# Optimization experiments

Measured on AMD Instinct MI355X. Metric: run time of the kernel, lower is better.

## Reference

```python
import jax, jax.numpy as jnp
import numpy as np

EPS = 1e-5

def conv2d(x, w, b, stride, pad):
    out = jax.lax.conv_general_dilated(x, w, (stride, stride), [(pad, pad), (pad, pad)],
                                       dimension_numbers=('NCHW', 'OIHW', 'NCHW'))
    return out + b[None, :, None, None]

def instance_norm(x):
    # nn.InstanceNorm2d default: affine=False, eps=1e-5, per (N,C) over (H,W)
    m = jnp.mean(x, axis=(2, 3), keepdims=True)
    v = jnp.var(x, axis=(2, 3), keepdims=True)
    return (x - m) * jax.lax.rsqrt(v + EPS)

def deform_conv2d(x, offset, mask, w, b, stride, pad):
    # x: [N,Cin,H,W]; offset: [N,2K,Ho,Wo] as [dy(K);dx(K)]; mask: [N,K,Ho,Wo]
    N, Cin, H, W = x.shape
    Cout, _, kh, kw = w.shape
    K = kh * kw
    Ho, Wo = mask.shape[2], mask.shape[3]
    oy, ox = offset[:, :K], offset[:, K:]
    ky, kx = jnp.meshgrid(jnp.arange(kh), jnp.arange(kw), indexing='ij')
    ky = ky.reshape(K).astype(x.dtype)
    kx = kx.reshape(K).astype(x.dtype)
    base_y = (jnp.arange(Ho) * stride - pad).astype(x.dtype)
    base_x = (jnp.arange(Wo) * stride - pad).astype(x.dtype)
    # sampling coords [N,K,Ho,Wo]
    py = base_y[None, None, :, None] + ky[None, :, None, None] + oy
    px = base_x[None, None, None, :] + kx[None, :, None, None] + ox
    y0 = jnp.floor(py)
    x0 = jnp.floor(px)
    wy = (py - y0)[:, None]  # [N,1,K,Ho,Wo]
    wx = (px - x0)[:, None]
    flat = x.reshape(N, Cin, H * W)

    def sample(yi, xi):
        valid = ((yi >= 0) & (yi <= H - 1) & (xi >= 0) & (xi <= W - 1)).astype(x.dtype)
        yc = jnp.clip(yi, 0, H - 1).astype(jnp.int32)
        xc = jnp.clip(xi, 0, W - 1).astype(jnp.int32)
        idx = yc * W + xc  # [N,K,Ho,Wo]
        vals = jax.vmap(lambda f, i: f[:, i])(flat, idx)  # [N,Cin,K,Ho,Wo]
        return vals * valid[:, None]

    v00 = sample(y0, x0)
    v01 = sample(y0, x0 + 1)
    v10 = sample(y0 + 1, x0)
    v11 = sample(y0 + 1, x0 + 1)
    samp = (v00 * (1 - wy) * (1 - wx) + v01 * (1 - wy) * wx
            + v10 * wy * (1 - wx) + v11 * wy * wx)
    samp = samp * mask[:, None]  # modulated (DCNv2)
    out = jnp.einsum('nckhw,ock->nohw', samp, w.reshape(Cout, Cin, K))
    return out + b[None, :, None, None]

def mdcp(x, off_w, off_b, dcn_w, dcn_b, stride, pad):
    # ModulatedDeformConvPack.forward with input_offset == input_real == x
    o = conv2d(x, off_w, off_b, stride, pad)
    K = o.shape[1] // 3
    o1, o2, m = o[:, :K], o[:, K:2 * K], o[:, 2 * K:]
    offset = jnp.concatenate([o1, o2], axis=1)
    mask = jax.nn.sigmoid(m)
    return deform_conv2d(x, offset, mask, dcn_w, dcn_b, stride, pad)

def res_block(x, w1, b1, w2, b2):
    # MUNIT-style ResBlock: [reflect-pad conv3x3, IN, ReLU] -> [reflect-pad conv3x3, IN] + skip
    h = jnp.pad(x, ((0, 0), (0, 0), (1, 1), (1, 1)), mode='reflect')
    h = jax.nn.relu(instance_norm(conv2d(h, w1, b1, 1, 0)))
    h = jnp.pad(h, ((0, 0), (0, 0), (1, 1), (1, 1)), mode='reflect')
    h = instance_norm(conv2d(h, w2, b2, 1, 0))
    return x + h

def setup_inputs() -> dict:
    key = jax.random.key(0)
    ks = jax.random.split(key, 32)
    N, H, W = 2, 256, 256

    def wconv(k, shape, scale=None):
        if scale is None:
            scale = 1.0 / np.sqrt(shape[1] * shape[2] * shape[3])
        return jax.random.normal(k, shape, jnp.float32) * scale

    def bias(k, n, scale=0.01):
        return jax.random.normal(k, (n,), jnp.float32) * scale

    inp = {}
    inp['x'] = jax.random.normal(ks[0], (N, 3, H, W), jnp.float32)
    # offset/mask convs: small weights (sub-pixel offsets; trained-from-zero in original)
    inp['off1_w'] = wconv(ks[1], (147, 3, 7, 7), 0.01)
    inp['off1_b'] = bias(ks[2], 147)
    inp['dcn1_w'] = wconv(ks[3], (64, 3, 7, 7))
    inp['dcn1_b'] = bias(ks[4], 64)
    inp['off2_w'] = wconv(ks[5], (48, 64, 4, 4), 0.01)
    inp['off2_b'] = bias(ks[6], 48)
    inp['dcn2_w'] = wconv(ks[7], (128, 64, 4, 4))
    inp['dcn2_b'] = bias(ks[8], 128)
    inp['off3_w'] = wconv(ks[9], (48, 128, 4, 4), 0.01)
    inp['off3_b'] = bias(ks[10], 48)
    inp['dcn3_w'] = wconv(ks[11], (256, 128, 4, 4))
    inp['dcn3_b'] = bias(ks[12], 256)
    for i, base in ((1, 13), (2, 17)):
        inp[f'rb{i}_w1'] = wconv(ks[base], (256, 256, 3, 3))
        inp[f'rb{i}_b1'] = bias(ks[base + 1], 256)
        inp[f'rb{i}_w2'] = wconv(ks[base + 2], (256, 256, 3, 3))
        inp[f'rb{i}_b2'] = bias(ks[base + 3], 256)
    return inp

def reference(x, off1_w, off1_b, dcn1_w, dcn1_b, off2_w, off2_b, dcn2_w, dcn2_b,
              off3_w, off3_b, dcn3_w, dcn3_b,
              rb1_w1, rb1_b1, rb1_w2, rb1_b2, rb2_w1, rb2_b1, rb2_w2, rb2_b2):
    h = jax.nn.relu(instance_norm(mdcp(x, off1_w, off1_b, dcn1_w, dcn1_b, 1, 3)))
    skip1 = h
    h = jax.nn.relu(instance_norm(mdcp(h, off2_w, off2_b, dcn2_w, dcn2_b, 2, 1)))
    skip2 = h
    h = jax.nn.relu(instance_norm(mdcp(h, off3_w, off3_b, dcn3_w, dcn3_b, 2, 1)))
    h = res_block(h, rb1_w1, rb1_b1, rb1_w2, rb1_b2)
    h = res_block(h, rb2_w1, rb2_b1, rb2_w2, rb2_b2)
    return (h, skip1, skip2)
```

## Files before the change

kernel.cpp:

```cpp
#include <hip/hip_runtime.h>
#include <hip/hip_bf16.h>
#include <math.h>

#define TPB 256
typedef __hip_bfloat16 bf16;
typedef short bf16x8 __attribute__((ext_vector_type(8)));
typedef float f32x4 __attribute__((ext_vector_type(4)));

constexpr long BIASF  = 0;
constexpr long RB1W1T = 2048;
constexpr long RB1W2T = 591872;
constexpr long RB2W1T = 1181696;
constexpr long RB2W2T = 1771520;
constexpr long FB     = 2361344;
constexpr long WB1OT  = 2361344;
constexpr long WB1DT  = 2382956;
constexpr long WO2T   = 2392364;
constexpr long WB2T   = 2441516;
constexpr long WO3T   = 2572588;
constexpr long WB3T   = 2670892;
constexpr long OFFB   = 3221504;
constexpr long H3F    = 4458496;
constexpr long PSUM   = 5507072;
constexpr long PSQ    = 5515264;
constexpr long CLBUF  = 5523456;
constexpr long OFF1B = 0,   DCN1B = 147;
constexpr long OFF2B = 211, DCN2B = 259;
constexpr long OFF3B = 387, DCN3B = 435;
constexpr long RB1B1 = 691, RB1B2 = 947;
constexpr long RB2B1 = 1203, RB2B2 = 1459;

template<int BF>
__device__ __forceinline__ float ldT(const void* p, long i) {
    if (BF) {
        unsigned short h = ((const unsigned short*)p)[i];
        return __uint_as_float(((unsigned int)h) << 16);
    }
    return ((const float*)p)[i];
}
template<int BF>
__device__ __forceinline__ void stT(void* p, long i, float v) {
    if (BF) ((bf16*)p)[i] = __float2bfloat16(v);
    else    ((float*)p)[i] = v;
}
__device__ __forceinline__ float bitsToF(unsigned short h) {
    return __uint_as_float(((unsigned int)h) << 16);
}
__device__ __forceinline__ unsigned short fToBits(float v) {
    bf16 h = __float2bfloat16(v);
    return *(unsigned short*)&h;
}

__global__ void detect_kernel(const void* __restrict__ x, int* __restrict__ flag) {
    if (threadIdx.x == 0 && blockIdx.x == 0) {
        const unsigned short* u = (const unsigned short*)x;
        int sane = 0;
        for (int i = 0; i < 256; ++i) {
            float v = bitsToF(u[i]);
            float a = fabsf(v);
            if (a > 0.0009f && a < 1100.f) ++sane;
        }
        *flag = (sane >= 224) ? 1 : 0;
    }
}

struct PtrPack { const void* p[20]; };

template<int BF>
__device__ void repack_all_body(PtrPack pp, float* __restrict__ fw)
{
    constexpr int  bcum  [11] = {0,147,211,259,387,435,691,947,1203,1459,1715};
    int j0 = blockIdx.x * 1024 + threadIdx.x * 4;
    #pragma unroll
    for (int q = 0; q < 4; ++q) {
        int j = j0 + q;
        if (j < 1715) {
            int v = 0;
            #pragma unroll
            for (int s = 1; s < 10; ++s) if (j >= bcum[s]) v = s;
            fw[BIASF + j] = ldT<BF>(pp.p[10 + v], j - bcum[v]);
        }
    }
}
__global__ __launch_bounds__(TPB) void repack_all_kernel(
    PtrPack pp, float* fw, const int* dflag) {
    if (*dflag) repack_all_body<1>(pp, fw);
    else        repack_all_body<0>(pp, fw);
}

__global__ __launch_bounds__(TPB) void repack_dcn_kernel(
    const void* __restrict__ w2, const void* __restrict__ w3,
    const void* __restrict__ w1o, const void* __restrict__ w1d,
    const void* __restrict__ w2o, const void* __restrict__ w3o,
    float* __restrict__ fw, const int* __restrict__ dflag)
{
    int bf = *dflag;
    unsigned short* wb2 = (unsigned short*)(fw + WB2T);
    unsigned short* wb3 = (unsigned short*)(fw + WB3T);
    unsigned short* wb1o = (unsigned short*)(fw + WB1OT);
    unsigned short* wb1d = (unsigned short*)(fw + WB1DT);
    unsigned short* wb2o = (unsigned short*)(fw + WO2T);
    unsigned short* wb3o = (unsigned short*)(fw + WO3T);
    int b = blockIdx.x;
    if (b < 128) {
        int e0 = b * 1024 + threadIdx.x * 4;
        #pragma unroll
        for (int j = 0; j < 4; ++j) {
            int e = e0 + j;
            int co = e >> 10, rem = e & 1023, k = rem >> 6, ci = rem & 63;
            long si = ((long)(co * 64 + ci)) * 16 + k;
            float v = bf ? ldT<1>(w2, si) : ldT<0>(w2, si);
            wb2[e] = fToBits(v);
        }
    } else if (b < 640) {
        int e0 = (b - 128) * 1024 + threadIdx.x * 4;
        #pragma unroll
        for (int j = 0; j < 4; ++j) {
            int e = e0 + j;
            int co = e >> 11, rem = e & 2047, k = rem >> 7, ci = rem & 127;
            long si = ((long)(co * 128 + ci)) * 16 + k;
            float v = bf ? ldT<1>(w3, si) : ldT<0>(w3, si);
            wb3[e] = fToBits(v);
        }
    } else if (b < 665) {
        int e0 = (b - 640) * 1024 + threadIdx.x * 4;
        #pragma unroll
        for (int j = 0; j < 4; ++j) {
            int e = e0 + j;
            int co = e / 160, k = e - co * 160;
            float v = 0.f;
            if (co < 147 && k < 147) {
                long si = (long)co * 147 + k;
                v = bf ? ldT<1>(w1o, si) : ldT<0>(w1o, si);
            }
            wb1o[e] = fToBits(v);
        }
    } else if (b < 675) {
        int e0 = (b - 665) * 1024 + threadIdx.x * 4;
        #pragma unroll
        for (int j = 0; j < 4; ++j) {
            int e = e0 + j;
            int co = e / 160, k = e - co * 160;
            float v = 0.f;
            if (k < 147) {
                long si = (long)co * 147 + k;
                v = bf ? ldT<1>(w1d, si) : ldT<0>(w1d, si);
            }
            wb1d[e] = fToBits(v);
        }
    } else if (b < 739) {
        int e0 = (b - 675) * 1024 + threadIdx.x * 4;
        #pragma unroll
        for (int j = 0; j < 4; ++j) {
            int e = e0 + j;
            int co = e >> 10, rem = e & 1023, k = rem >> 6, ci = rem & 63;
            float v = 0.f;
            if (co < 48) {
                long si = ((long)(co * 64 + ci)) * 16 + k;
                v = bf ? ldT<1>(w2o, si) : ldT<0>(w2o, si);
            }
            wb2o[e] = fToBits(v);
        }
    } else {
        int e0 = (b - 739) * 1024 + threadIdx.x * 4;
        #pragma unroll
        for (int j = 0; j < 4; ++j) {
            int e = e0 + j;
            int co = e >> 11, rem = e & 2047, k = rem >> 7, ci = rem & 127;
            float v = 0.f;
            if (co < 48) {
                long si = ((long)(co * 128 + ci)) * 16 + k;
                v = bf ? ldT<1>(w3o, si) : ldT<0>(w3o, si);
            }
            wb3o[e] = fToBits(v);
        }
    }
}

struct RbPack { const void* src[4]; };
__global__ __launch_bounds__(TPB) void repack_rb_kernel(
    RbPack rp, float* fw, const int* dflag)
{
    __shared__ unsigned short lw[4 * 2304];
    int b = blockIdx.x;
    int ten = b >> 6;
    int co0 = (b & 63) * 4;
    const void* src = rp.src[ten];
    const long dstOff[4] = {RB1W1T, RB1W2T, RB2W1T, RB2W2T};
    unsigned short* dst = (unsigned short*)(fw + dstOff[ten]);
    int bf = *dflag;
    int t = threadIdx.x;
    for (int e = t; e < 4 * 2304; e += TPB) {
        int coL = e / 2304, i = e - coL * 2304;
        long si = (long)(co0 + coL) * 2304 + i;
        float v = bf ? ldT<1>(src, si) : ldT<0>(src, si);
        lw[e] = fToBits(v);
    }
    __syncthreads();
    for (int e = t; e < 9216; e += TPB) {
        int ci = e & 255, coL = (e >> 8) & 3, q = e >> 10;
        dst[((long)q * 256 + co0 + coL) * 256 + ci] = lw[coL * 2304 + ci * 9 + q];
    }
}

template<int BF>
__device__ void x_to_cl4_body(const void* __restrict__ x, unsigned short* __restrict__ x4)
{
    long gid = (long)blockIdx.x * TPB + threadIdx.x;
    int n = (int)(gid >> 16); int p = (int)(gid & 65535);
    long xb = (long)n * 3 * 65536 + p;
    unsigned c0 = fToBits(ldT<BF>(x, xb));
    unsigned c1 = fToBits(ldT<BF>(x, xb + 65536));
    unsigned c2 = fToBits(ldT<BF>(x, xb + 131072));
    uint2 v; v.x = c0 | (c1 << 16); v.y = c2;
    *(uint2*)&x4[gid * 4] = v;
}
__global__ __launch_bounds__(TPB) void x_to_cl4_kernel(
    const void* x, unsigned short* x4, const int* dflag)
{
    if (*dflag) x_to_cl4_body<1>(x, x4);
    else        x_to_cl4_body<0>(x, x4);
}

template<int BF>
__device__ void layer1_mfma_body(
    const unsigned short* __restrict__ x4all, const unsigned short* __restrict__ wo,
    const unsigned short* __restrict__ wd, const float* __restrict__ bias1,
    const float* __restrict__ bias2, void* __restrict__ out, long obase,
    float* xs, unsigned short* A, float* offs)
{
    int b = blockIdx.x;
    int n = b >> 11;
    int ho = (b >> 3) & 255;
    int wo0 = (b & 7) << 5;
    const unsigned short* x4 = x4all + ((long)n << 16) * 4;
    int t = threadIdx.x;

    for (int e = t; e < 7 * 40; e += TPB) {
        int cc = e % 40, rr = e / 40;
        int yy = ho - 3 + rr; int xx = wo0 - 3 + cc;
        float c0 = 0.f, c1 = 0.f, c2 = 0.f;
        if (cc < 38 && yy >= 0 && yy < 256 && xx >= 0 && xx < 256) {
            uint2 v = *(const uint2*)&x4[((long)yy * 256 + xx) * 4];
            c0 = bitsToF((unsigned short)(v.x & 0xffff));
            c1 = bitsToF((unsigned short)(v.x >> 16));
            c2 = bitsToF((unsigned short)(v.y & 0xffff));
        }
        xs[(0 * 7 + rr) * 40 + cc] = c0;
        xs[(1 * 7 + rr) * 40 + cc] = c1;
        xs[(2 * 7 + rr) * 40 + cc] = c2;
    }
    __syncthreads();

    for (int e = t; e < 5120; e += TPB) {
        int kin = e & 31, m = (e >> 5) & 31, kc = e >> 10;
        int k = kc * 32 + kin;
        float v = 0.f;
        if (k < 147) {
            int ci = k / 49, q = k - ci * 49;
            int ky = q / 7, kx = q - ky * 7;
            v = xs[(ci * 7 + ky) * 40 + m + kx];
        }
        A[kc * 1024 + m * 32 + kin] = fToBits(v);
    }
    __syncthreads();

    int wv = t >> 6, lane = t & 63;
    int quad = lane >> 4, l16 = lane & 15;
    int mt = wv & 1, ntb = wv >> 1;

    {
        f32x4 acc[5];
        #pragma unroll
        for (int j = 0; j < 5; ++j) acc[j] = (f32x4){0.f, 0.f, 0.f, 0.f};
        #pragma unroll
        for (int kc = 0; kc < 5; ++kc) {
            bf16x8 a = *(const bf16x8*)&A[(kc * 32 + mt * 16 + l16) * 32 + quad * 8];
            #pragma unroll
            for (int j = 0; j < 5; ++j) {
                int ch = (ntb + 2 * j) * 16 + l16;
                bf16x8 bw = *(const bf16x8*)&wo[ch * 160 + kc * 32 + quad * 8];
                acc[j] = __builtin_amdgcn_mfma_f32_16x16x32_bf16(a, bw, acc[j], 0, 0, 0);
            }
        }
        #pragma unroll
        for (int j = 0; j < 5; ++j) {
            int ch = (ntb + 2 * j) * 16 + l16;
            if (ch < 147) {
                float bv = bias1[ch];
                #pragma unroll
                for (int reg = 0; reg < 4; ++reg) {
                    int m = mt * 16 + quad * 4 + reg;
                    offs[ch * 33 + m] = acc[j][reg] + bv;
                }
            }
        }
    }
    __syncthreads();

    for (int e = t; e < 49 * 32; e += TPB) {
        int p = e & 31; int k = e >> 5;
        float oy = offs[k * 33 + p];
        float ox = offs[(49 + k) * 33 + p];
        float mr = offs[(98 + k) * 33 + p];
        float m = 1.f / (1.f + expf(-mr));
        float py = (float)(ho - 3 + k / 7) + oy;
        float px = (float)(wo0 + p - 3 + k % 7) + ox;
        float y0f = floorf(py), x0f = floorf(px);
        float wy = py - y0f, wx = px - x0f;
        int y0 = (int)y0f, x0 = (int)x0f;
        bool yv0 = (y0 >= 0) && (y0 < 256);
        bool yv1 = (y0 + 1 >= 0) && (y0 + 1 < 256);
        bool xv0 = (x0 >= 0) && (x0 < 256);
        bool xv1 = (x0 + 1 >= 0) && (x0 + 1 < 256);
        int y0c = min(max(y0, 0), 255), y1c = min(max(y0 + 1, 0), 255);
        int x0c = min(max(x0, 0), 255), x1c = min(max(x0 + 1, 0), 255);
        float w00 = (yv0 && xv0) ? (1.f - wy) * (1.f - wx) * m : 0.f;
        float w01 = (yv0 && xv1) ? (1.f - wy) * wx * m : 0.f;
        float w10 = (yv1 && xv0) ? wy * (1.f - wx) * m : 0.f;
        float w11 = (yv1 && xv1) ? wy * wx * m : 0.f;
        uint2 a00 = *(const uint2*)&x4[((long)y0c * 256 + x0c) * 4];
        uint2 a01 = *(const uint2*)&x4[((long)y0c * 256 + x1c) * 4];
        uint2 a10 = *(const uint2*)&x4[((long)y1c * 256 + x0c) * 4];
        uint2 a11 = *(const uint2*)&x4[((long)y1c * 256 + x1c) * 4];
        float s0 = w00 * bitsToF((unsigned short)(a00.x & 0xffff))
                 + w01 * bitsToF((unsigned short)(a01.x & 0xffff))
                 + w10 * bitsToF((unsigned short)(a10.x & 0xffff))
                 + w11 * bitsToF((unsigned short)(a11.x & 0xffff));
        float s1 = w00 * bitsToF((unsigned short)(a00.x >> 16))
                 + w01 * bitsToF((unsigned short)(a01.x >> 16))
                 + w10 * bitsToF((unsigned short)(a10.x >> 16))
                 + w11 * bitsToF((unsigned short)(a11.x >> 16));
        float s2 = w00 * bitsToF((unsigned short)(a00.y & 0xffff))
                 + w01 * bitsToF((unsigned short)(a01.y & 0xffff))
                 + w10 * bitsToF((unsigned short)(a10.y & 0xffff))
                 + w11 * bitsToF((unsigned short)(a11.y & 0xffff));
        offs[k * 33 + p] = s0;
        offs[(49 + k) * 33 + p] = s1;
        offs[(98 + k) * 33 + p] = s2;
    }
    __syncthreads();

    for (int e = t; e < 5120; e += TPB) {
        int kin = e & 31, m = (e >> 5) & 31, kc = e >> 10;
        int k = kc * 32 + kin;
        float v = 0.f;
        if (k < 147) v = offs[k * 33 + m];
        A[kc * 1024 + m * 32 + kin] = fToBits(v);
    }
    __syncthreads();

    f32x4 acc2[2];
    acc2[0] = (f32x4){0.f, 0.f, 0.f, 0.f};
    acc2[1] = (f32x4){0.f, 0.f, 0.f, 0.f};
    #pragma unroll
    for (int kc = 0; kc < 5; ++kc) {
        bf16x8 a = *(const bf16x8*)&A[(kc * 32 + mt * 16 + l16) * 32 + quad * 8];
        #pragma unroll
        for (int j = 0; j < 2; ++j) {
            int co = (ntb + 2 * j) * 16 + l16;
            bf16x8 bw = *(const bf16x8*)&wd[co * 160 + kc * 32 + quad * 8];
            acc2[j] = __builtin_amdgcn_mfma_f32_16x16x32_bf16(a, bw, acc2[j], 0, 0, 0);
        }
    }
    #pragma unroll
    for (int j = 0; j < 2; ++j) {
        int co = (ntb + 2 * j) * 16 + l16;
        float bv = bias2[co];
        #pragma unroll
        for (int reg = 0; reg < 4; ++reg) {
            int wox = wo0 + mt * 16 + quad * 4 + reg;
            long oi = obase + ((long)(n * 64 + co) * 256 + ho) * 256 + wox;
            stT<BF>(out, oi, acc2[j][reg] + bv);
        }
    }
}

__global__ __launch_bounds__(TPB) void layer1_mfma_kernel(
    const unsigned short* x4, const unsigned short* wo, const unsigned short* wd,
    const float* bias1, const float* bias2, void* out, long obase, const int* dflag)
{
    __shared__ __align__(16) float xs[3 * 7 * 40];
    __shared__ __align__(16) unsigned short A[5120];
    __shared__ __align__(16) float offs[147 * 33];
    if (*dflag) layer1_mfma_body<1>(x4, wo, wd, bias1, bias2, out, obase, xs, A, offs);
    else        layer1_mfma_body<0>(x4, wo, wd, bias1, bias2, out, obase, xs, A, offs);
}

template<int CIN, int HH, int WW, int HO, int WO>
__global__ __launch_bounds__(TPB) void offconv_mfma_kernel(
    const unsigned short* __restrict__ xcl, const unsigned short* __restrict__ wb,
    const float* __restrict__ bias_f, float* __restrict__ out)
{
    constexpr int S   = 16 * CIN;
    constexpr int KL  = 512 / CIN;
    constexpr int NCH = 16 / KL;
    constexpr int PAIRS_W = (KL * 16) / 4;
    constexpr int TILES = (HO * WO) / 16;

    __shared__ int tp[256];
    __shared__ __align__(16) unsigned short smp[16 * 512];

    int tile = blockIdx.x % TILES;
    int n    = blockIdx.x / TILES;
    int lp0  = tile * 16;

    {
        int pr = threadIdx.x;
        int k = pr >> 4, p = pr & 15;
        int lp = lp0 + p;
        int ho = lp / WO, wo = lp - ho * WO;
        int yy = ho * 2 - 1 + (k >> 2);
        int xx = wo * 2 - 1 + (k & 3);
        bool valid = (yy >= 0) && (yy < HH) && (xx >= 0) && (xx < WW);
        tp[pr] = valid ? (yy * WW + xx) * CIN : -1;
    }

    int wv = threadIdx.x >> 6, lane = threadIdx.x & 63;
    int quad = lane >> 4, l16 = lane & 15;
    const unsigned short* xn = xcl + (long)n * HH * WW * CIN;

    f32x4 acc = (f32x4){0.f, 0.f, 0.f, 0.f};

    for (int ch = 0; ch < NCH; ++ch) {
        __syncthreads();
        #pragma unroll 4
        for (int u = 0; u < PAIRS_W; ++u) {
            int prl = wv * PAIRS_W + u;
            int pi  = ch * (KL * 16) + prl;
            int kl = prl >> 4, p = prl & 15;
            int t0 = tp[pi];
            #pragma unroll
            for (int cg = 0; cg < CIN / 64; ++cg) {
                int ci = cg * 64 + lane;
                unsigned short v = (t0 >= 0) ? xn[t0 + ci] : (unsigned short)0;
                int il = kl * CIN + ci;
                smp[((il >> 5) * 16 + p) * 32 + (il & 31)] = v;
            }
        }
        __syncthreads();
        #pragma unroll 4
        for (int kk = 0; kk < 16; ++kk) {
            bf16x8 a = *(const bf16x8*)&smp[(kk * 16 + l16) * 32 + quad * 8];
            int co = wv * 16 + l16;
            bf16x8 b = *(const bf16x8*)&wb[(long)co * S + ch * 512 + kk * 32 + quad * 8];
            acc = __builtin_amdgcn_mfma_f32_16x16x32_bf16(a, b, acc, 0, 0, 0);
        }
    }

    int co = wv * 16 + l16;
    if (co < 48) {
        float bv = bias_f[co];
        #pragma unroll
        for (int reg = 0; reg < 4; ++reg) {
            int lp = lp0 + quad * 4 + reg;
            int ho = lp / WO, wo = lp - ho * WO;
            out[((long)(n * 48 + co) * HO + ho) * WO + wo] = acc[reg] + bv;
        }
    }
}

template<int C>
__global__ __launch_bounds__(TPB) void nchw_to_cl_kernel(
    const void* __restrict__ in, long ibase, unsigned short* __restrict__ out,
    int HW, const int* __restrict__ dflag)
{
    __shared__ unsigned short tile[C * 65];
    int bf = *dflag;
    int n   = (blockIdx.x * 64) / HW;
    int px0 = (blockIdx.x * 64) % HW;
    for (int e = threadIdx.x; e < C * 64; e += TPB) {
        int c = e >> 6, p = e & 63;
        long si = ibase + (long)(n * C + c) * HW + px0 + p;
        float v = bf ? ldT<1>(in, si) : ldT<0>(in, si);
        tile[c * 65 + p] = fToBits(v);
    }
    __syncthreads();
    for (int e = threadIdx.x; e < C * 64; e += TPB) {
        int p = e / C, c = e - p * C;
        out[((long)n * HW + px0 + p) * C + c] = tile[c * 65 + p];
    }
}

template<int MODE, int CIN, int COUT, int NWAVES, int HH, int WW, int HO, int WO>
__global__ __launch_bounds__(NWAVES * 64) void deform_mfma_kernel(
    const unsigned short* __restrict__ xcl, const float* __restrict__ off,
    const unsigned short* __restrict__ wb, const float* __restrict__ bias_f,
    void* __restrict__ outp, long obase, const int* __restrict__ dflag)
{
    constexpr int TPBk = NWAVES * 64;
    constexpr int S    = 16 * CIN;
    constexpr int KL   = 512 / CIN;
    constexpr int NCH  = 16 / KL;
    constexpr int CH2  = CIN / 2;
    constexpr int ITER = (KL * 16 * CH2) / TPBk;
    constexpr int TILES = (HO * WO) / 16;

    __shared__ __align__(16) int tpw[256][8];
    __shared__ __align__(16) unsigned short smp[16 * 512];

    int tile = blockIdx.x % TILES;
    int n    = blockIdx.x / TILES;
    int lp0  = tile * 16;
    int tid  = threadIdx.x;

    if (tid < 256) {
        int pr = tid;
        int k = pr >> 4, p = pr & 15;
        int lp = lp0 + p;
        int ho = lp / WO, wo = lp - ho * WO;
        long plane = (long)HO * WO;
        const float* offn = off + (long)n * 48 * plane;
        float oy = offn[(long)k * plane + lp];
        float ox = offn[(long)(16 + k) * plane + lp];
        float mr = offn[(long)(32 + k) * plane + lp];
        float m = 1.f / (1.f + expf(-mr));
        float py = (float)(ho * 2 - 1 + (k >> 2)) + oy;
        float px = (float)(wo * 2 - 1 + (k & 3)) + ox;
        float y0f = floorf(py), x0f = floorf(px);
        float wy = py - y0f, wx = px - x0f;
        int y0 = (int)y0f, x0 = (int)x0f;
        bool yv0 = (y0 >= 0) && (y0 < HH);
        bool yv1 = (y0 + 1 >= 0) && (y0 + 1 < HH);
        bool xv0 = (x0 >= 0) && (x0 < WW);
        bool xv1 = (x0 + 1 >= 0) && (x0 + 1 < WW);
        int y0c = min(max(y0, 0), HH - 1), y1c = min(max(y0 + 1, 0), HH - 1);
        int x0c = min(max(x0, 0), WW - 1), x1c = min(max(x0 + 1, 0), WW - 1);
        tpw[pr][0] = (y0c * WW + x0c) * CIN;
        tpw[pr][1] = (y0c * WW + x1c) * CIN;
        tpw[pr][2] = (y1c * WW + x0c) * CIN;
        tpw[pr][3] = (y1c * WW + x1c) * CIN;
        tpw[pr][4] = __float_as_int((yv0 && xv0) ? (1.f - wy) * (1.f - wx) * m : 0.f);
        tpw[pr][5] = __float_as_int((yv0 && xv1) ? (1.f - wy) * wx * m : 0.f);
        tpw[pr][6] = __float_as_int((yv1 && xv0) ? wy * (1.f - wx) * m : 0.f);
        tpw[pr][7] = __float_as_int((yv1 && xv1) ? wy * wx * m : 0.f);
    }

    int wv = tid >> 6, lane = tid & 63;
    int quad = lane >> 4, l16 = lane & 15;
    int cb = (wv & 3) * 32 + (wv >> 2) * (COUT / 2);
    const unsigned short* xn = xcl + (long)n * HH * WW * CIN;

    f32x4 acc[2];
    acc[0] = (f32x4){0.f, 0.f, 0.f, 0.f};
    acc[1] = (f32x4){0.f, 0.f, 0.f, 0.f};

    for (int ch = 0; ch < NCH; ++ch) {
        __syncthreads();
        #pragma unroll 4
        for (int it = 0; it < ITER; ++it) {
            int e   = it * TPBk + tid;
            int prl = e / CH2;
            int ci  = (e - prl * CH2) * 2;
            int pi  = ch * (KL * 16) + prl;
            const int4   tp4 = *(const int4*)&tpw[pi][0];
            const float4 tw4 = *(const float4*)&tpw[pi][4];
            unsigned v0 = *(const unsigned*)(xn + tp4.x + ci);
            unsigned v1 = *(const unsigned*)(xn + tp4.y + ci);
            unsigned v2 = *(const unsigned*)(xn + tp4.z + ci);
            unsigned v3 = *(const unsigned*)(xn + tp4.w + ci);
            float r0 = tw4.x * bitsToF((unsigned short)(v0 & 0xffff))
                     + tw4.y * bitsToF((unsigned short)(v1 & 0xffff))
                     + tw4.z * bitsToF((unsigned short)(v2 & 0xffff))
                     + tw4.w * bitsToF((unsigned short)(v3 & 0xffff));
            float r1 = tw4.x * bitsToF((unsigned short)(v0 >> 16))
                     + tw4.y * bitsToF((unsigned short)(v1 >> 16))
                     + tw4.z * bitsToF((unsigned short)(v2 >> 16))
                     + tw4.w * bitsToF((unsigned short)(v3 >> 16));
            unsigned ov = (unsigned)fToBits(r0) | ((unsigned)fToBits(r1) << 16);
            int il = (prl >> 4) * CIN + ci;
            int p  = prl & 15;
            *(unsigned*)&smp[((il >> 5) * 16 + p) * 32 + (il & 31)] = ov;
        }
        __syncthreads();
        #pragma unroll 4
        for (int kk = 0; kk < 16; ++kk) {
            bf16x8 a = *(const bf16x8*)&smp[(kk * 16 + l16) * 32 + quad * 8];
            #pragma unroll
            for (int f = 0; f < 2; ++f) {
                int co = cb + f * 16 + l16;
                bf16x8 b = *(const bf16x8*)&wb[(long)co * S + ch * 512 + kk * 32 + quad * 8];
                acc[f] = __builtin_amdgcn_mfma_f32_16x16x32_bf16(a, b, acc[f], 0, 0, 0);
            }
        }
    }

    if (MODE == 1) {
        unsigned short* oCL = (unsigned short*)outp;
        #pragma unroll
        for (int f = 0; f < 2; ++f) {
            int co = cb + f * 16 + l16;
            float bv = bias_f[co];
            #pragma unroll
            for (int reg = 0; reg < 4; ++reg) {
                int lp = lp0 + quad * 4 + reg;
                oCL[((long)n * HO * WO + lp) * COUT + co] = fToBits(acc[f][reg] + bv);
            }
        }
    } else {
        int bf = *dflag;
        #pragma unroll
        for (int f = 0; f < 2; ++f) {
            int co = cb + f * 16 + l16;
            float bv = bias_f[co];
            #pragma unroll
            for (int reg = 0; reg < 4; ++reg) {
                int lp = lp0 + quad * 4 + reg;
                int ho = lp / WO, wo = lp - ho * WO;
                long oi = obase + ((long)(n * COUT + co) * HO + ho) * WO + wo;
                if (bf) stT<1>(outp, oi, acc[f][reg] + bv);
                else    stT<0>(outp, oi, acc[f][reg] + bv);
            }
        }
    }
}

__global__ __launch_bounds__(TPB) void resconv_mfma_kernel(
    const unsigned short* __restrict__ X, const unsigned short* __restrict__ W,
    const float* __restrict__ bias_f, bf16* __restrict__ Y)
{
    __shared__ __align__(16) unsigned short xs[3 * 66 * 64];
    int b = blockIdx.x;
    int coO = b & 7, r = (b >> 3) & 63, n = b >> 9;
    int t = threadIdx.x;
    int wv = t >> 6;
    int lane = t & 63;
    int quad = lane >> 4, l16 = lane & 15;
    int rows[3];
    rows[0] = (r == 0) ? 1 : r - 1;
    rows[1] = r;
    rows[2] = (r == 63) ? 62 : r + 1;

    f32x4 acc[2];
    acc[0] = (f32x4){0.f, 0.f, 0.f, 0.f};
    acc[1] = (f32x4){0.f, 0.f, 0.f, 0.f};

    long xbase = (long)n * 4096 * 256;

    for (int ci0 = 0; ci0 < 256; ci0 += 64) {
        __syncthreads();
        for (int e = t; e < 3 * 66 * 8; e += TPB) {
            int oct = e & 7;
            int col = (e >> 3) % 66;
            int ky  = e / (66 * 8);
            int gx = col - 1;
            gx = (gx < 0) ? 1 : ((gx > 63) ? 62 : gx);
            bf16x8 v = *(const bf16x8*)&X[xbase + ((long)rows[ky] * 64 + gx) * 256 + ci0 + oct * 8];
            int slot = oct ^ (col & 7);
            *(bf16x8*)&xs[((ky * 66 + col) << 6) + slot * 8] = v;
        }
        __syncthreads();
        #pragma unroll
        for (int q = 0; q < 9; ++q) {
            int ky = q / 3, kx = q % 3;
            int col = wv * 16 + l16 + kx;
            int base = (ky * 66 + col) << 6;
            #pragma unroll
            for (int kh = 0; kh < 2; ++kh) {
                int slot = (kh * 4 + quad) ^ (col & 7);
                bf16x8 a = *(const bf16x8*)&xs[base + slot * 8];
                #pragma unroll
                for (int ct = 0; ct < 2; ++ct) {
                    int co = coO * 32 + ct * 16 + l16;
                    bf16x8 bw = *(const bf16x8*)&W[((long)q * 256 + co) * 256 + ci0 + kh * 32 + quad * 8];
                    acc[ct] = __builtin_amdgcn_mfma_f32_16x16x32_bf16(a, bw, acc[ct], 0, 0, 0);
                }
            }
        }
    }

    long ybase = ((long)n * 4096 + (long)r * 64) * 256;
    #pragma unroll
    for (int ct = 0; ct < 2; ++ct) {
        int co = coO * 32 + ct * 16 + l16;
        float bv = bias_f[co];
        #pragma unroll
        for (int reg = 0; reg < 4; ++reg) {
            int px = wv * 16 + quad * 4 + reg;
            Y[ybase + (long)px * 256 + co] = __float2bfloat16(acc[ct][reg] + bv);
        }
    }
}

__global__ __launch_bounds__(TPB) void cl_stats_kernel(
    const unsigned short* __restrict__ X, float* __restrict__ psum, float* __restrict__ psq)
{
    int blk = blockIdx.x;
    int chunk = blk & 15, n = blk >> 4;
    int co = threadIdx.x;
    float s = 0.f, sq = 0.f;
    const unsigned short* p = X + ((long)n * 4096 + chunk * 256) * 256 + co;
    for (int i = 0; i < 256; ++i) {
        float v = bitsToF(p[(long)i * 256]);
        s += v; sq += v * v;
    }
    psum[(n * 16 + chunk) * 256 + co] = s;
    psq [(n * 16 + chunk) * 256 + co] = sq;
}

__device__ __forceinline__ void cl_load_stats(
    const float* psum, const float* psq, int n, float* mv, float* iv)
{
    int t = threadIdx.x;
    float s = 0.f, sq = 0.f;
    for (int c = 0; c < 16; ++c) {
        s  += psum[(n * 16 + c) * 256 + t];
        sq += psq [(n * 16 + c) * 256 + t];
    }
    float mean = s / 4096.f;
    mv[t] = mean;
    iv[t] = rsqrtf(sq / 4096.f - mean * mean + 1e-5f);
    __syncthreads();
}

__global__ __launch_bounds__(TPB) void cl_apply_kernel(
    unsigned short* __restrict__ X, const float* __restrict__ psum,
    const float* __restrict__ psq, int relu)
{
    __shared__ float mv[256], iv[256];
    int y = blockIdx.x & 63, n = blockIdx.x >> 6;
    cl_load_stats(psum, psq, n, mv, iv);
    unsigned short* row = X + ((long)n * 4096 + y * 64) * 256;
    for (int e = threadIdx.x; e < 64 * 256; e += TPB) {
        int co = e & 255;
        float v = (bitsToF(row[e]) - mv[co]) * iv[co];
        if (relu) v = fmaxf(v, 0.f);
        row[e] = fToBits(v);
    }
}

__global__ __launch_bounds__(TPB) void cl_apply_add_kernel(
    const unsigned short* __restrict__ T, unsigned short* __restrict__ H,
    const float* __restrict__ psum, const float* __restrict__ psq)
{
    __shared__ float mv[256], iv[256];
    int y = blockIdx.x & 63, n = blockIdx.x >> 6;
    cl_load_stats(psum, psq, n, mv, iv);
    long base = ((long)n * 4096 + y * 64) * 256;
    for (int e = threadIdx.x; e < 64 * 256; e += TPB) {
        int co = e & 255;
        float v = bitsToF(H[base + e]) + (bitsToF(T[base + e]) - mv[co]) * iv[co];
        H[base + e] = fToBits(v);
    }
}

__global__ __launch_bounds__(TPB) void cl_apply_final_kernel(
    const unsigned short* __restrict__ T, const unsigned short* __restrict__ H,
    void* __restrict__ outp, const float* __restrict__ psum,
    const float* __restrict__ psq, const int* __restrict__ dflag)
{
    __shared__ float mv[256], iv[256];
    int y = blockIdx.x & 63, n = blockIdx.x >> 6;
    cl_load_stats(psum, psq, n, mv, iv);
    int bf = *dflag;
    int x = threadIdx.x & 63, cg = threadIdx.x >> 6;
    for (int co = cg; co < 256; co += 4) {
        long cli = ((long)(n * 64 + y) * 64 + x) * 256 + co;
        float v = bitsToF(H[cli]) + (bitsToF(T[cli]) - mv[co]) * iv[co];
        long oi = (((long)(n * 256 + co)) * 64 + y) * 64 + x;
        if (bf) ((bf16*)outp)[oi] = __float2bfloat16(v);
        else    ((float*)outp)[oi] = v;
    }
}

__device__ __forceinline__ void reduce2(float& sum, float& sq, float* s1, float* s2)
{
    for (int off = 32; off; off >>= 1) {
        sum += __shfl_down(sum, off, 64);
        sq  += __shfl_down(sq,  off, 64);
    }
    int nw = blockDim.x >> 6;
    int wid = threadIdx.x >> 6;
    if ((threadIdx.x & 63) == 0) { s1[wid] = sum; s2[wid] = sq; }
    __syncthreads();
    sum = 0.f; sq = 0.f;
    for (int w = 0; w < nw; ++w) { sum += s1[w]; sq += s2[w]; }
}

__global__ void instnorm_kernel(
    void* __restrict__ buf, long base0, const int* __restrict__ dflag,
    int HW, int relu)
{
    __shared__ float s1[16], s2[16];
    int bf = *dflag;
    long base = base0 + (long)blockIdx.x * HW;
    float sum = 0.f, sq = 0.f;
    for (int i = threadIdx.x; i < HW; i += blockDim.x) {
        float v = bf ? bitsToF(((const unsigned short*)buf)[base + i])
                     : ((const float*)buf)[base + i];
        sum += v; sq += v * v;
    }
    reduce2(sum, sq, s1, s2);
    float mean = sum / HW;
    float inv = rsqrtf(sq / HW - mean * mean + 1e-5f);
    for (int i = threadIdx.x; i < HW; i += blockDim.x) {
        float v = bf ? bitsToF(((const unsigned short*)buf)[base + i])
                     : ((const float*)buf)[base + i];
        v = (v - mean) * inv;
        if (relu) v = fmaxf(v, 0.f);
        if (bf) ((bf16*)buf)[base + i] = __float2bfloat16(v);
        else    ((float*)buf)[base + i] = v;
    }
}

extern "C" void kernel_launch(void* const* d_in, const int* in_sizes, int n_in,
                              void* d_out, int out_size, void* d_ws, size_t ws_size,
                              hipStream_t stream) {
    const void* x = d_in[0];

    const long SKIP1 = 2097152;
    const long SKIP2 = 10485760;

    int* dflag = (int*)d_ws;
    float* fw = (float*)((char*)d_ws + 64);

    unsigned short* t1 = (unsigned short*)(fw + FB);
    unsigned short* t2 = (unsigned short*)(fw + FB + 1048576);
    unsigned short* h3 = (unsigned short*)(fw + H3F);
    float* offb = fw + OFFB;
    unsigned short* x4 = (unsigned short*)(fw + OFFB);
    float* psum = fw + PSUM;
    float* psq  = fw + PSQ;
    unsigned short* clbuf = (unsigned short*)(fw + CLBUF);
    const unsigned short* wb1o = (const unsigned short*)(fw + WB1OT);
    const unsigned short* wb1d = (const unsigned short*)(fw + WB1DT);
    const unsigned short* wb2o = (const unsigned short*)(fw + WO2T);
    const unsigned short* wb3o = (const unsigned short*)(fw + WO3T);
    const unsigned short* wb2 = (const unsigned short*)(fw + WB2T);
    const unsigned short* wb3 = (const unsigned short*)(fw + WB3T);
    const unsigned short* rbw1 = (const unsigned short*)(fw + RB1W1T);
    const unsigned short* rbw2 = (const unsigned short*)(fw + RB1W2T);
    const unsigned short* rbw3 = (const unsigned short*)(fw + RB2W1T);
    const unsigned short* rbw4 = (const unsigned short*)(fw + RB2W2T);

    detect_kernel<<<1, 64, 0, stream>>>(x, dflag);

    PtrPack pp;
    for (int i = 0; i < 10; ++i) pp.p[i] = nullptr;
    pp.p[10] = d_in[2];  pp.p[11] = d_in[4];  pp.p[12] = d_in[6];  pp.p[13] = d_in[8];
    pp.p[14] = d_in[10]; pp.p[15] = d_in[12]; pp.p[16] = d_in[14]; pp.p[17] = d_in[16];
    pp.p[18] = d_in[18]; pp.p[19] = d_in[20];
    repack_all_kernel<<<2, TPB, 0, stream>>>(pp, fw, dflag);
    repack_dcn_kernel<<<867, TPB, 0, stream>>>(
        d_in[7], d_in[11], d_in[1], d_in[3], d_in[5], d_in[9], fw, dflag);
    RbPack rp;
    rp.src[0] = d_in[13]; rp.src[1] = d_in[15]; rp.src[2] = d_in[17]; rp.src[3] = d_in[19];
    repack_rb_kernel<<<256, TPB, 0, stream>>>(rp, fw, dflag);

    x_to_cl4_kernel<<<512, TPB, 0, stream>>>(x, x4, dflag);
    layer1_mfma_kernel<<<4096, TPB, 0, stream>>>(
        x4, wb1o, wb1d, fw + OFF1B, fw + DCN1B, d_out, SKIP1, dflag);
    instnorm_kernel<<<128, 1024, 0, stream>>>(d_out, SKIP1, dflag, 65536, 1);
    nchw_to_cl_kernel<64><<<2048, TPB, 0, stream>>>(d_out, SKIP1, clbuf, 65536, dflag);

    offconv_mfma_kernel<64, 256, 256, 128, 128><<<2048, TPB, 0, stream>>>(
        clbuf, wb2o, fw + OFF2B, offb);
    deform_mfma_kernel<0, 64, 128, 4, 256, 256, 128, 128><<<2048, TPB, 0, stream>>>(
        clbuf, offb, wb2, fw + DCN2B, d_out, SKIP2, dflag);
    instnorm_kernel<<<256, 512, 0, stream>>>(d_out, SKIP2, dflag, 16384, 1);
    nchw_to_cl_kernel<128><<<512, TPB, 0, stream>>>(d_out, SKIP2, clbuf, 16384, dflag);

    offconv_mfma_kernel<128, 128, 128, 64, 64><<<512, TPB, 0, stream>>>(
        clbuf, wb3o, fw + OFF3B, offb);
    deform_mfma_kernel<1, 128, 256, 8, 128, 128, 64, 64><<<512, 512, 0, stream>>>(
        clbuf, offb, wb3, fw + DCN3B, h3, 0, dflag);
    cl_stats_kernel<<<32, TPB, 0, stream>>>(h3, psum, psq);
    cl_apply_kernel<<<128, TPB, 0, stream>>>(h3, psum, psq, 1);

    resconv_mfma_kernel<<<1024, TPB, 0, stream>>>(h3, rbw1, fw + RB1B1, (bf16*)t1);
    cl_stats_kernel<<<32, TPB, 0, stream>>>(t1, psum, psq);
    cl_apply_kernel<<<128, TPB, 0, stream>>>(t1, psum, psq, 1);
    resconv_mfma_kernel<<<1024, TPB, 0, stream>>>(t1, rbw2, fw + RB1B2, (bf16*)t2);
    cl_stats_kernel<<<32, TPB, 0, stream>>>(t2, psum, psq);
    cl_apply_add_kernel<<<128, TPB, 0, stream>>>(t2, h3, psum, psq);

    resconv_mfma_kernel<<<1024, TPB, 0, stream>>>(h3, rbw3, fw + RB2B1, (bf16*)t1);
    cl_stats_kernel<<<32, TPB, 0, stream>>>(t1, psum, psq);
    cl_apply_kernel<<<128, TPB, 0, stream>>>(t1, psum, psq, 1);
    resconv_mfma_kernel<<<1024, TPB, 0, stream>>>(t1, rbw4, fw + RB2B2, (bf16*)t2);
    cl_stats_kernel<<<32, TPB, 0, stream>>>(t2, psum, psq);
    cl_apply_final_kernel<<<128, TPB, 0, stream>>>(t2, h3, d_out, psum, psq, dflag);
}
```

Baseline: 894.0 us.

## Fuse instance-norm partial statistics into conv epilogues and vectorize apply kernels

The per-channel sum and sum-of-squares partials are now computed in the epilogues of the layer-3 deform conv and the resblock convs, using wave shuffles. A small finalize kernel turns them into mean and inverse std. This removes the separate stats kernels that re-read the whole bf16 activation with only 32 blocks. The apply kernels now process two bf16 values per 32-bit access. The price is extra partial buffers and a serial 256-step reduction in finalize, and statistics are taken from fp32 values before bf16 rounding.

```diff
diff --git a/kernel.cpp b/kernel.cpp
--- a/kernel.cpp
+++ b/kernel.cpp
@@ -24,6 +24,8 @@
 constexpr long PSUM   = 5507072;
 constexpr long PSQ    = 5515264;
 constexpr long CLBUF  = 5523456;
+constexpr long PPART  = 7620608;
+constexpr long QPART  = 7751680;
 constexpr long OFF1B = 0,   DCN1B = 147;
 constexpr long OFF2B = 211, DCN2B = 259;
 constexpr long OFF3B = 387, DCN3B = 435;
@@ -486,7 +488,8 @@
 __global__ __launch_bounds__(NWAVES * 64) void deform_mfma_kernel(
     const unsigned short* __restrict__ xcl, const float* __restrict__ off,
     const unsigned short* __restrict__ wb, const float* __restrict__ bias_f,
-    void* __restrict__ outp, long obase, const int* __restrict__ dflag)
+    void* __restrict__ outp, long obase, const int* __restrict__ dflag,
+    float* __restrict__ P, float* __restrict__ Q)
 {
     constexpr int TPBk = NWAVES * 64;
     constexpr int S    = 16 * CIN;
@@ -591,10 +594,20 @@
         for (int f = 0; f < 2; ++f) {
             int co = cb + f * 16 + l16;
             float bv = bias_f[co];
+            float s = 0.f, q = 0.f;
             #pragma unroll
             for (int reg = 0; reg < 4; ++reg) {
                 int lp = lp0 + quad * 4 + reg;
-                oCL[((long)n * HO * WO + lp) * COUT + co] = fToBits(acc[f][reg] + bv);
+                float v = acc[f][reg] + bv;
+                oCL[((long)n * HO * WO + lp) * COUT + co] = fToBits(v);
+                s += v; q += v * v;
+            }
+            s += __shfl_down(s, 16, 64); s += __shfl_down(s, 32, 64);
+            q += __shfl_down(q, 16, 64); q += __shfl_down(q, 32, 64);
+            if (lane < 16) {
+                int row = (int)blockIdx.x * 8 + wv;
+                P[row * 32 + f * 16 + l16] = s;
+                Q[row * 32 + f * 16 + l16] = q;
             }
         }
     } else {
@@ -617,7 +630,8 @@
 
 __global__ __launch_bounds__(TPB) void resconv_mfma_kernel(
     const unsigned short* __restrict__ X, const unsigned short* __restrict__ W,
-    const float* __restrict__ bias_f, bf16* __restrict__ Y)
+    const float* __restrict__ bias_f, bf16* __restrict__ Y,
+    float* __restrict__ P, float* __restrict__ Q)
 {
     __shared__ __align__(16) unsigned short xs[3 * 66 * 64];
     int b = blockIdx.x;
@@ -674,86 +688,106 @@
     for (int ct = 0; ct < 2; ++ct) {
         int co = coO * 32 + ct * 16 + l16;
         float bv = bias_f[co];
+        float s = 0.f, q = 0.f;
         #pragma unroll
         for (int reg = 0; reg < 4; ++reg) {
             int px = wv * 16 + quad * 4 + reg;
-            Y[ybase + (long)px * 256 + co] = __float2bfloat16(acc[ct][reg] + bv);
-        }
-    }
-}
-
-__global__ __launch_bounds__(TPB) void cl_stats_kernel(
-    const unsigned short* __restrict__ X, float* __restrict__ psum, float* __restrict__ psq)
-{
-    int blk = blockIdx.x;
-    int chunk = blk & 15, n = blk >> 4;
-    int co = threadIdx.x;
-    float s = 0.f, sq = 0.f;
-    const unsigned short* p = X + ((long)n * 4096 + chunk * 256) * 256 + co;
-    for (int i = 0; i < 256; ++i) {
-        float v = bitsToF(p[(long)i * 256]);
-        s += v; sq += v * v;
-    }
-    psum[(n * 16 + chunk) * 256 + co] = s;
-    psq [(n * 16 + chunk) * 256 + co] = sq;
-}
-
-__device__ __forceinline__ void cl_load_stats(
-    const float* psum, const float* psq, int n, float* mv, float* iv)
-{
-    int t = threadIdx.x;
-    float s = 0.f, sq = 0.f;
-    for (int c = 0; c < 16; ++c) {
-        s  += psum[(n * 16 + c) * 256 + t];
-        sq += psq [(n * 16 + c) * 256 + t];
+            float v = acc[ct][reg] + bv;
+            Y[ybase + (long)px * 256 + co] = __float2bfloat16(v);
+            s += v; q += v * v;
+        }
+        s += __shfl_down(s, 16, 64); s += __shfl_down(s, 32, 64);
+        q += __shfl_down(q, 16, 64); q += __shfl_down(q, 32, 64);
+        if (lane < 16) {
+            int row = (b << 2) | wv;
+            P[row * 32 + ct * 16 + l16] = s;
+            Q[row * 32 + ct * 16 + l16] = q;
+        }
+    }
+}
+
+template<int MODE>
+__global__ __launch_bounds__(256) void cl_finalize_kernel(
+    const float* __restrict__ P, const float* __restrict__ Q,
+    float* __restrict__ mvz, float* __restrict__ ivz)
+{
+    int n = blockIdx.x, co = threadIdx.x;
+    float s = 0.f, q = 0.f;
+    if (MODE == 0) {
+        int coO = co >> 5, col = co & 31;
+        for (int j = 0; j < 256; ++j) {
+            int r = j >> 2, wv = j & 3;
+            int row = ((((n << 9) | (r << 3) | coO)) << 2) | wv;
+            s += P[row * 32 + col]; q += Q[row * 32 + col];
+        }
+    } else {
+        int wvf = ((co >> 7) << 2) | ((co >> 5) & 3);
+        int col = co & 31;
+        for (int tile = 0; tile < 256; ++tile) {
+            int row = (((n << 8) | tile) << 3) | wvf;
+            s += P[row * 32 + col]; q += Q[row * 32 + col];
+        }
     }
     float mean = s / 4096.f;
-    mv[t] = mean;
-    iv[t] = rsqrtf(sq / 4096.f - mean * mean + 1e-5f);
-    __syncthreads();
+    mvz[n * 256 + co] = mean;
+    ivz[n * 256 + co] = rsqrtf(q / 4096.f - mean * mean + 1e-5f);
 }
 
 __global__ __launch_bounds__(TPB) void cl_apply_kernel(
-    unsigned short* __restrict__ X, const float* __restrict__ psum,
-    const float* __restrict__ psq, int relu)
+    unsigned short* __restrict__ X, const float* __restrict__ mvz,
+    const float* __restrict__ ivz, int relu)
 {
     __shared__ float mv[256], iv[256];
     int y = blockIdx.x & 63, n = blockIdx.x >> 6;
-    cl_load_stats(psum, psq, n, mv, iv);
-    unsigned short* row = X + ((long)n * 4096 + y * 64) * 256;
-    for (int e = threadIdx.x; e < 64 * 256; e += TPB) {
-        int co = e & 255;
-        float v = (bitsToF(row[e]) - mv[co]) * iv[co];
-        if (relu) v = fmaxf(v, 0.f);
-        row[e] = fToBits(v);
+    int t = threadIdx.x;
+    mv[t] = mvz[n * 256 + t]; iv[t] = ivz[n * 256 + t];
+    __syncthreads();
+    unsigned* row = (unsigned*)(X + ((long)n * 4096 + y * 64) * 256);
+    for (int e = t; e < 8192; e += TPB) {
+        int co = (e * 2) & 255;
+        unsigned u = row[e];
+        float v0 = (bitsToF((unsigned short)(u & 0xffff)) - mv[co]) * iv[co];
+        float v1 = (bitsToF((unsigned short)(u >> 16)) - mv[co + 1]) * iv[co + 1];
+        if (relu) { v0 = fmaxf(v0, 0.f); v1 = fmaxf(v1, 0.f); }
+        row[e] = (unsigned)fToBits(v0) | ((unsigned)fToBits(v1) << 16);
     }
 }
 
 __global__ __launch_bounds__(TPB) void cl_apply_add_kernel(
     const unsigned short* __restrict__ T, unsigned short* __restrict__ H,
-    const float* __restrict__ psum, const float* __restrict__ psq)
+    const float* __restrict__ mvz, const float* __restrict__ ivz)
 {
     __shared__ float mv[256], iv[256];
     int y = blockIdx.x & 63, n = blockIdx.x >> 6;
-    cl_load_stats(psum, psq, n, mv, iv);
+    int t = threadIdx.x;
+    mv[t] = mvz[n * 256 + t]; iv[t] = ivz[n * 256 + t];
+    __syncthreads();
     long base = ((long)n * 4096 + y * 64) * 256;
-    for (int e = threadIdx.x; e < 64 * 256; e += TPB) {
-        int co = e & 255;
-        float v = bitsToF(H[base + e]) + (bitsToF(T[base + e]) - mv[co]) * iv[co];
-        H[base + e] = fToBits(v);
+    const unsigned* tr = (const unsigned*)(T + base);
+    unsigned* hr = (unsigned*)(H + base);
+    for (int e = t; e < 8192; e += TPB) {
+        int co = (e * 2) & 255;
+        unsigned ut = tr[e], uh = hr[e];
+        float v0 = bitsToF((unsigned short)(uh & 0xffff))
+                 + (bitsToF((unsigned short)(ut & 0xffff)) - mv[co]) * iv[co];
+        float v1 = bitsToF((unsigned short)(uh >> 16))
+                 + (bitsToF((unsigned short)(ut >> 16)) - mv[co + 1]) * iv[co + 1];
+        hr[e] = (unsigned)fToBits(v0) | ((unsigned)fToBits(v1) << 16);
     }
 }
 
 __global__ __launch_bounds__(TPB) void cl_apply_final_kernel(
     const unsigned short* __restrict__ T, const unsigned short* __restrict__ H,
-    void* __restrict__ outp, const float* __restrict__ psum,
-    const float* __restrict__ psq, const int* __restrict__ dflag)
+    void* __restrict__ outp, const float* __restrict__ mvz,
+    const float* __restrict__ ivz, const int* __restrict__ dflag)
 {
     __shared__ float mv[256], iv[256];
     int y = blockIdx.x & 63, n = blockIdx.x >> 6;
-    cl_load_stats(psum, psq, n, mv, iv);
+    int t = threadIdx.x;
+    mv[t] = mvz[n * 256 + t]; iv[t] = ivz[n * 256 + t];
+    __syncthreads();
     int bf = *dflag;
-    int x = threadIdx.x & 63, cg = threadIdx.x >> 6;
+    int x = t & 63, cg = t >> 6;
     for (int co = cg; co < 256; co += 4) {
         long cli = ((long)(n * 64 + y) * 64 + x) * 256 + co;
         float v = bitsToF(H[cli]) + (bitsToF(T[cli]) - mv[co]) * iv[co];
@@ -819,8 +853,10 @@
     unsigned short* h3 = (unsigned short*)(fw + H3F);
     float* offb = fw + OFFB;
     unsigned short* x4 = (unsigned short*)(fw + OFFB);
-    float* psum = fw + PSUM;
-    float* psq  = fw + PSQ;
+    float* mvz = fw + PSUM;
+    float* ivz = fw + PSQ;
+    float* P = fw + PPART;
+    float* Q = fw + QPART;
     unsigned short* clbuf = (unsigned short*)(fw + CLBUF);
     const unsigned short* wb1o = (const unsigned short*)(fw + WB1OT);
     const unsigned short* wb1d = (const unsigned short*)(fw + WB1DT);
@@ -856,28 +892,28 @@
     offconv_mfma_kernel<64, 256, 256, 128, 128><<<2048, TPB, 0, stream>>>(
         clbuf, wb2o, fw + OFF2B, offb);
     deform_mfma_kernel<0, 64, 128, 4, 256, 256, 128, 128><<<2048, TPB, 0, stream>>>(
-        clbuf, offb, wb2, fw + DCN2B, d_out, SKIP2, dflag);
+        clbuf, offb, wb2, fw + DCN2B, d_out, SKIP2, dflag, nullptr, nullptr);
     instnorm_kernel<<<256, 512, 0, stream>>>(d_out, SKIP2, dflag, 16384, 1);
     nchw_to_cl_kernel<128><<<512, TPB, 0, stream>>>(d_out, SKIP2, clbuf, 16384, dflag);
 
     offconv_mfma_kernel<128, 128, 128, 64, 64><<<512, TPB, 0, stream>>>(
         clbuf, wb3o, fw + OFF3B, offb);
     deform_mfma_kernel<1, 128, 256, 8, 128, 128, 64, 64><<<512, 512, 0, stream>>>(
-        clbuf, offb, wb3, fw + DCN3B, h3, 0, dflag);
-    cl_stats_kernel<<<32, TPB, 0, stream>>>(h3, psum, psq);
-    cl_apply_kernel<<<128, TPB, 0, stream>>>(h3, psum, psq, 1);
-
-    resconv_mfma_kernel<<<1024, TPB, 0, stream>>>(h3, rbw1, fw + RB1B1, (bf16*)t1);
-    cl_stats_kernel<<<32, TPB, 0, stream>>>(t1, psum, psq);
-    cl_apply_kernel<<<128, TPB, 0, stream>>>(t1, psum, psq, 1);
-    resconv_mfma_kernel<<<1024, TPB, 0, stream>>>(t1, rbw2, fw + RB1B2, (bf16*)t2);
-    cl_stats_kernel<<<32, TPB, 0, stream>>>(t2, psum, psq);
-    cl_apply_add_kernel<<<128, TPB, 0, stream>>>(t2, h3, psum, psq);
-
-    resconv_mfma_kernel<<<1024, TPB, 0, stream>>>(h3, rbw3, fw + RB2B1, (bf16*)t1);
-    cl_stats_kernel<<<32, TPB, 0, stream>>>(t1, psum, psq);
-    cl_apply_kernel<<<128, TPB, 0, stream>>>(t1, psum, psq, 1);
-    resconv_mfma_kernel<<<1024, TPB, 0, stream>>>(t1, rbw4, fw + RB2B2, (bf16*)t2);
-    cl_stats_kernel<<<32, TPB, 0, stream>>>(t2, psum, psq);
-    cl_apply_final_kernel<<<128, TPB, 0, stream>>>(t2, h3, d_out, psum, psq, dflag);
-}
+        clbuf, offb, wb3, fw + DCN3B, h3, 0, dflag, P, Q);
+    cl_finalize_kernel<1><<<2, 256, 0, stream>>>(P, Q, mvz, ivz);
+    cl_apply_kernel<<<128, TPB, 0, stream>>>(h3, mvz, ivz, 1);
+
+    resconv_mfma_kernel<<<1024, TPB, 0, stream>>>(h3, rbw1, fw + RB1B1, (bf16*)t1, P, Q);
+    cl_finalize_kernel<0><<<2, 256, 0, stream>>>(P, Q, mvz, ivz);
+    cl_apply_kernel<<<128, TPB, 0, stream>>>(t1, mvz, ivz, 1);
+    resconv_mfma_kernel<<<1024, TPB, 0, stream>>>(t1, rbw2, fw + RB1B2, (bf16*)t2, P, Q);
+    cl_finalize_kernel<0><<<2, 256, 0, stream>>>(P, Q, mvz, ivz);
+    cl_apply_add_kernel<<<128, TPB, 0, stream>>>(t2, h3, mvz, ivz);
+
+    resconv_mfma_kernel<<<1024, TPB, 0, stream>>>(h3, rbw3, fw + RB2B1, (bf16*)t1, P, Q);
+    cl_finalize_kernel<0><<<2, 256, 0, stream>>>(P, Q, mvz, ivz);
+    cl_apply_kernel<<<128, TPB, 0, stream>>>(t1, mvz, ivz, 1);
+    resconv_mfma_kernel<<<1024, TPB, 0, stream>>>(t1, rbw4, fw + RB2B2, (bf16*)t2, P, Q);
+    cl_finalize_kernel<0><<<2, 256, 0, stream>>>(P, Q, mvz, ivz);
+    cl_apply_final_kernel<<<128, TPB, 0, stream>>>(t2, h3, d_out, mvz, ivz, dflag);
+}
```

Result: slower. 931.6 us (+4.2%).
